# Performance work log

Measured on AMD Instinct MI355X. Metric: run time of the kernel, lower is better.

Reference implementation:

```python
import jax, jax.numpy as jnp
import numpy as np
import math

TAU = 0.5        # module stores self.tau = 1.0 / tau with tau=2.0
THRESHOLD = 1.0
SURR_C = 1.0 / (2.0 * math.sqrt(2.0 * math.pi))  # coefficient in Stochastic.backward


@jax.custom_vjp
def spike(v):
    # Stochastic.forward: (input > 0).float()
    return (v > 0).astype(v.dtype)


def _spike_fwd(v):
    return spike(v), v


def _spike_bwd(v, g):
    # Stochastic.backward: grad * 1/(2*sqrt(2*pi)) * exp(-v^2/2)
    return (g * (SURR_C * jnp.exp(-0.5 * v * v)),)


spike.defvjp(_spike_fwd, _spike_bwd)


def setup_inputs() -> dict:
    key = jax.random.key(0)
    x = jax.random.normal(key, (32, 128, 8192), dtype=jnp.float32)  # [B, T, N]
    return {"x": x}


def reference(x):
    # Eval-mode iterative stochastic-LIF update (no noise injection).
    xt = jnp.swapaxes(x, 0, 1)  # [T, B, N] for scan over time

    def step(u, x_t):
        u = TAU * u + x_t                # leaky integrate
        o = spike(u - THRESHOLD)         # fire
        u = u * (1.0 - o)                # hard reset by multiply
        return u, o

    u0 = jnp.zeros_like(xt[0])
    _, o = jax.lax.scan(step, u0, xt)
    return jnp.swapaxes(o, 0, 1)  # [B, T, N]
```

## Files before the change

kernel.cpp:

```cpp
#include <hip/hip_runtime.h>
#include <stdint.h>


constexpr int B  = 32;
constexpr int T  = 128;
constexpr int N  = 8192;
constexpr int THREADS = 256;
constexpr int NTILES  = N / THREADS;
constexpr int DP      = 16;

__global__ __launch_bounds__(THREADS) void lif_kernel(const float* __restrict__ x,
                                                      float* __restrict__ out) {
    const int tid   = threadIdx.x;
    const int b     = blockIdx.x >> 5;
    const int ntile = blockIdx.x & (NTILES - 1);
    const uint32_t base = (uint32_t)b * (T * N) + (uint32_t)ntile * THREADS + tid;
    const float* gx = x + base;
    float*       go = out + base;

    float pipe[DP];
    #pragma unroll
    for (int k = 0; k < DP; ++k) pipe[k] = gx[(uint32_t)k * N];

    float u = 0.f;
    uint32_t sw0 = 0u, sw1 = 0u, sw2 = 0u, sw3 = 0u;

    #pragma unroll
    for (int t = 0; t < T; ++t) {
        const float v = pipe[t & (DP - 1)];
        if (t + DP < T)
            pipe[t & (DP - 1)] = gx[(uint32_t)(t + DP) * N];
        u = 0.5f * u + v;
        const bool s = u > 1.0f;
        const uint32_t bit = s ? 1u : 0u;
        if      (t <  32) sw0 |= bit << t;
        else if (t <  64) sw1 |= bit << (t - 32);
        else if (t <  96) sw2 |= bit << (t - 64);
        else              sw3 |= bit << (t - 96);
        u = s ? 0.0f : u;
    }

    #pragma unroll
    for (int t = 0; t < T; ++t) {
        const uint32_t w = (t < 32) ? sw0 : (t < 64) ? sw1 : (t < 96) ? sw2 : sw3;
        const float sp = ((w >> (t & 31)) & 1u) ? 1.0f : 0.0f;
        __builtin_nontemporal_store(sp, go + (uint32_t)t * N);
    }
}

extern "C" void kernel_launch(void* const* d_in, const int* in_sizes, int n_in,
                              void* d_out, int out_size, void* d_ws, size_t ws_size,
                              hipStream_t stream) {
    const float* x   = (const float*)d_in[0];
    float*       out = (float*)d_out;
    lif_kernel<<<B * NTILES, THREADS, 0, stream>>>(x, out);
}
```

Measured before the change: 232.0 us.

## Split LIF into bit-packed scan kernel and parallel expand kernel via workspace

The fused kernel becomes two kernels when workspace is available. The first scans over time and writes 128 spike bits per neuron as a uint4 to workspace. The second expands those bits to floats, with each block covering 4 timesteps across 8192 neurons. The aim is to separate the serial, read-heavy scan phase from the write-heavy output phase so each has better memory behaviour, at the cost of an extra launch and a small workspace round trip.

Result: slower. 241.2 us (+4.0%).

```diff
diff --git a/kernel.cpp b/kernel.cpp
--- a/kernel.cpp
+++ b/kernel.cpp
@@ -8,6 +8,69 @@
 constexpr int THREADS = 256;
 constexpr int NTILES  = N / THREADS;
 constexpr int DP      = 16;
+constexpr size_t WS_NEEDED = (size_t)B * N * 16;
+
+__global__ __launch_bounds__(THREADS) void scan_kernel(const float* __restrict__ x,
+                                                       uint4* __restrict__ ws4) {
+    const int tid   = threadIdx.x;
+    const int b     = blockIdx.x >> 5;
+    const int ntile = blockIdx.x & (NTILES - 1);
+    const uint32_t base = (uint32_t)b * (T * N) + (uint32_t)ntile * THREADS + tid;
+    const float* gx = x + base;
+
+    float pipe[DP];
+    #pragma unroll
+    for (int k = 0; k < DP; ++k) pipe[k] = gx[(uint32_t)k * N];
+
+    float u = 0.f;
+    uint32_t sw0 = 0u, sw1 = 0u, sw2 = 0u, sw3 = 0u;
+
+    #pragma unroll
+    for (int t = 0; t < T; ++t) {
+        const float v = pipe[t & (DP - 1)];
+        if (t + DP < T)
+            pipe[t & (DP - 1)] = gx[(uint32_t)(t + DP) * N];
+        u = 0.5f * u + v;
+        const bool s = u > 1.0f;
+        const uint32_t bit = s ? 1u : 0u;
+        if      (t <  32) sw0 |= bit << t;
+        else if (t <  64) sw1 |= bit << (t - 32);
+        else if (t <  96) sw2 |= bit << (t - 64);
+        else              sw3 |= bit << (t - 96);
+        u = s ? 0.0f : u;
+    }
+
+    const uint32_t chain = (uint32_t)b * N + (uint32_t)ntile * THREADS + tid;
+    ws4[chain] = make_uint4(sw0, sw1, sw2, sw3);
+}
+
+__global__ __launch_bounds__(THREADS) void expand_kernel(const uint4* __restrict__ ws4,
+                                                         float* __restrict__ out) {
+    const int tid = threadIdx.x;
+    const int b   = blockIdx.x >> 5;
+    const int tg  = blockIdx.x & 31;
+    const uint4* src = ws4 + (uint32_t)b * N;
+    float* dst = out + (size_t)b * (T * N) + (size_t)tg * 4 * N;
+    const int w  = tg >> 3;
+    const int s0 = (tg & 7) * 4;
+
+    uint32_t pw[32];
+    #pragma unroll
+    for (int i = 0; i < 32; ++i) {
+        const uint4 p = src[(uint32_t)i * THREADS + tid];
+        pw[i] = (w == 0) ? p.x : (w == 1) ? p.y : (w == 2) ? p.z : p.w;
+    }
+
+    #pragma unroll
+    for (int dt = 0; dt < 4; ++dt) {
+        float* row = dst + (size_t)dt * N;
+        #pragma unroll
+        for (int i = 0; i < 32; ++i) {
+            const float f = ((pw[i] >> (s0 + dt)) & 1u) ? 1.0f : 0.0f;
+            __builtin_nontemporal_store(f, row + (uint32_t)i * THREADS + tid);
+        }
+    }
+}
 
 __global__ __launch_bounds__(THREADS) void lif_kernel(const float* __restrict__ x,
                                                       float* __restrict__ out) {
@@ -42,8 +105,8 @@
 
     #pragma unroll
     for (int t = 0; t < T; ++t) {
-        const uint32_t w = (t < 32) ? sw0 : (t < 64) ? sw1 : (t < 96) ? sw2 : sw3;
-        const float sp = ((w >> (t & 31)) & 1u) ? 1.0f : 0.0f;
+        const uint32_t wd = (t < 32) ? sw0 : (t < 64) ? sw1 : (t < 96) ? sw2 : sw3;
+        const float sp = ((wd >> (t & 31)) & 1u) ? 1.0f : 0.0f;
         __builtin_nontemporal_store(sp, go + (uint32_t)t * N);
     }
 }
@@ -53,5 +116,12 @@
                               hipStream_t stream) {
     const float* x   = (const float*)d_in[0];
     float*       out = (float*)d_out;
-    lif_kernel<<<B * NTILES, THREADS, 0, stream>>>(x, out);
+    const int nblocks = B * NTILES;
+    if (d_ws != nullptr && ws_size >= WS_NEEDED) {
+        uint4* ws4 = (uint4*)d_ws;
+        scan_kernel<<<nblocks, THREADS, 0, stream>>>(x, ws4);
+        expand_kernel<<<nblocks, THREADS, 0, stream>>>(ws4, out);
+    } else {
+        lif_kernel<<<nblocks, THREADS, 0, stream>>>(x, out);
+    }
 }
```
